# Performance work log

Hardware: AMD Instinct MI355X
Metric: run time of the kernel (lower is better)

## Reference

```python
import jax, jax.numpy as jnp
import numpy as np

D_MODEL = 4096
D_FIBER = 16
D_CONTROL = 64
EMA_MOMENTUM = 0.9


def setup_inputs() -> dict:
    key = jax.random.key(0)
    k_h, k_f, k_w1, k_w2 = jax.random.split(key, 4)
    B, S = 4, 2048
    hidden = jax.random.normal(k_h, (B, S, D_MODEL), dtype=jnp.float32)
    # torch nn.Linear stores weight as [out, in]; fiber_proj init: normal std=0.02
    W_fiber = jax.random.normal(k_f, (D_FIBER, D_MODEL), dtype=jnp.float32) * 0.02
    # predictor[0]: Linear(d_model+d_fiber, d_control) with default torch init (uniform)
    fan_in1 = D_MODEL + D_FIBER
    bound1 = 1.0 / np.sqrt(fan_in1)
    W1 = jax.random.uniform(k_w1, (D_CONTROL, fan_in1), dtype=jnp.float32, minval=-bound1, maxval=bound1)
    b1 = jnp.zeros((D_CONTROL,), dtype=jnp.float32)
    # predictor[-2]: Linear(d_control, 1), weight normal std=0.01, bias zero
    W2 = jax.random.normal(k_w2, (1, D_CONTROL), dtype=jnp.float32) * 0.01
    b2 = jnp.zeros((1,), dtype=jnp.float32)
    lam = jnp.asarray(1.0, dtype=jnp.float32)
    return {"hidden": hidden, "W_fiber": W_fiber, "W1": W1, "b1": b1, "W2": W2, "b2": b2, "lam": lam}


def _causal_ema(delta_h, alpha):
    # h_t = alpha*h_{t-1} + (1-alpha)*d_t, h_{-1} = 0. delta_h: [B,S]
    B = delta_h.shape[0]
    def step(h_prev, d_t):
        h_t = alpha * h_prev + (1.0 - alpha) * d_t
        return h_t, h_t
    _, hs = jax.lax.scan(step, jnp.zeros((B,), delta_h.dtype), jnp.swapaxes(delta_h, 0, 1))
    return jnp.swapaxes(hs, 0, 1)  # [B,S]


def reference(hidden, W_fiber, W1, b1, W2, b2, lam):
    h = hidden.astype(jnp.float32)                      # [B,S,D]
    fiber = jnp.einsum('bsd,fd->bsf', h, W_fiber)       # [B,S,16]
    combined = jnp.concatenate([h, fiber], axis=-1)     # [B,S,D+16]
    z = jax.nn.gelu(jnp.einsum('bsc,kc->bsk', combined, W1) + b1, approximate=False)
    delta_h = jax.nn.softplus(jnp.einsum('bsk,ok->bso', z, W2) + b2)[..., 0]  # [B,S]
    field = _causal_ema(delta_h, EMA_MOMENTUM)          # [B,S]
    gate = jax.nn.sigmoid(-lam * field)
    return gate.astype(hidden.dtype), field.astype(hidden.dtype), delta_h.mean()
```

## Files before the change

kernel.cpp:

```cpp
#include <hip/hip_runtime.h>
#include <hip/hip_bf16.h>

#define D_MODEL 4096
#define NTOK    8192
#define SEQ     2048

typedef short bf16x8 __attribute__((ext_vector_type(8)));
typedef float f32x4  __attribute__((ext_vector_type(4)));

__device__ __forceinline__ short f2bf(float x) {
  __hip_bfloat16 h = __float2bfloat16(x);
  return *reinterpret_cast<short*>(&h);
}
__device__ __forceinline__ float bfs2f(unsigned short u) {
  unsigned int x = ((unsigned int)u) << 16;
  float f;
  __builtin_memcpy(&f, &x, 4);
  return f;
}
__device__ __forceinline__ float bf2f(const void* p, size_t i) {
  return bfs2f(((const unsigned short*)p)[i]);
}

__device__ __forceinline__ void gload_lds16(const void* g, void* l) {
  __builtin_amdgcn_global_load_lds(
      (__attribute__((address_space(1))) void*)(g),
      (__attribute__((address_space(3))) void*)(l), 16, 0, 0);
}

__device__ __forceinline__ int sniff_wave(const unsigned short* p, int n) {
  int lane = threadIdx.x & 63;
  int S = n / 2 < 64 ? n / 2 : 64;
  bool act = lane < S;
  unsigned short ve = 0, vo = 0;
  if (act) { ve = p[2 * lane]; vo = p[2 * lane + 1]; }
  int ee = (ve >> 7) & 0xFF, eo = (vo >> 7) & 0xFF;
  bool ve_band   = (ve == 0) || (ve == 0x8000) || (ee >= 96 && ee <= 141);
  bool vo_bandnz = (vo != 0) && (vo != 0x8000) && (eo >= 96 && eo <= 141);
  int zp = __popcll(__ballot(act && ve == 0 && vo == 0));
  int ob = __popcll(__ballot(act && ve == 0 && vo_bandnz));
  int eb = __popcll(__ballot(act && ve_band));
  if (zp == S) return 1;
  if (4 * ob >= 3 * S) return 0;
  if (4 * eb >= 3 * S) return 1;
  return 0;
}

__device__ __forceinline__ float decode_lam(const void* lamp) {
  unsigned short l0 = *(const unsigned short*)lamp;
  int le = (l0 >> 7) & 0xFF;
  if (l0 != 0 && l0 != 0x8000 && le >= 96 && le <= 141)
    return bfs2f(l0);
  return *(const float*)lamp;
}
__device__ __forceinline__ float decode_b2(const void* p) {
  unsigned short c0 = *(const unsigned short*)p;
  int ce = (c0 >> 7) & 0xFF;
  if (c0 == 0) return 0.0f;
  if (c0 != 0x8000 && ce >= 96 && ce <= 141)
    return bfs2f(c0);
  return *(const float*)p;
}

__global__ __launch_bounds__(256) void fold_w1(const void* __restrict__ W1v,
                                               const void* __restrict__ Wfv,
                                               short* __restrict__ W1eff) {
  int n = blockIdx.x;
  int fw1 = sniff_wave((const unsigned short*)W1v, 64 * 4112);
  int fwf = sniff_wave((const unsigned short*)Wfv, 16 * D_MODEL);
  __shared__ float w1b[16];
  if (threadIdx.x < 16) {
    size_t idx = (size_t)n * 4112 + 4096 + threadIdx.x;
    w1b[threadIdx.x] = fw1 ? bf2f(W1v, idx) : ((const float*)W1v)[idx];
  }
  __syncthreads();
  for (int it = 0; it < 4; ++it) {
    int k0 = it * 1024 + threadIdx.x * 4;
    size_t idx = (size_t)n * 4112 + k0;
    float v0, v1, v2, v3;
    if (fw1) {
      ushort4 u = *(const ushort4*)((const unsigned short*)W1v + idx);
      v0 = bfs2f(u.x); v1 = bfs2f(u.y); v2 = bfs2f(u.z); v3 = bfs2f(u.w);
    } else {
      float4 f = *(const float4*)((const float*)W1v + idx);
      v0 = f.x; v1 = f.y; v2 = f.z; v3 = f.w;
    }
#pragma unroll
    for (int f = 0; f < 16; ++f) {
      size_t wi = (size_t)f * D_MODEL + k0;
      float w0, w1_, w2_, w3_;
      if (fwf) {
        ushort4 u = *(const ushort4*)((const unsigned short*)Wfv + wi);
        w0 = bfs2f(u.x); w1_ = bfs2f(u.y); w2_ = bfs2f(u.z); w3_ = bfs2f(u.w);
      } else {
        float4 fv = *(const float4*)((const float*)Wfv + wi);
        w0 = fv.x; w1_ = fv.y; w2_ = fv.z; w3_ = fv.w;
      }
      float s = w1b[f];
      v0 += s * w0; v1 += s * w1_; v2 += s * w2_; v3 += s * w3_;
    }
    ushort4 o;
    o.x = (unsigned short)f2bf(v0); o.y = (unsigned short)f2bf(v1);
    o.z = (unsigned short)f2bf(v2); o.w = (unsigned short)f2bf(v3);
    *(ushort4*)(W1eff + (size_t)n * D_MODEL + k0) = o;
  }
}

__global__ __launch_bounds__(256, 2) void gemm_part(const void* __restrict__ hid,
                                                    const short* __restrict__ B_,
                                                    float* __restrict__ part) {
  int t = blockIdx.x >> 3;
  int c = blockIdx.x & 7;
  int w    = threadIdx.x >> 6;
  int lane = threadIdx.x & 63;
  int m = lane & 15, kg = lane >> 4;

  __shared__ short As[64 * 512];

  int fhid = sniff_wave((const unsigned short*)hid, NTOK * D_MODEL);

  f32x4 acc0 = {0.f, 0.f, 0.f, 0.f};
  f32x4 acc1 = acc0, acc2 = acc0, acc3 = acc0;

  const short* Bp = B_ + (size_t)m * D_MODEL + c * 512 + kg * 8;

  if (fhid) {
#pragma unroll
    for (int i = 0; i < 16; ++i) {
      int n = w * 16 + i;
      const char* src = (const char*)hid +
          ((size_t)(t * 64 + n) * D_MODEL + c * 512) * 2 +
          ((lane ^ (n & 7)) * 16);
      gload_lds16(src, (char*)As + n * 1024);
    }
    asm volatile("s_waitcnt vmcnt(0)" ::: "memory");
#pragma unroll
    for (int s = 0; s < 16; ++s) {
      int u  = s * 4 + kg;
      int row = w * 16 + m;
      bf16x8 a = *(const bf16x8*)((const char*)As + row * 1024 +
                                  ((u ^ (m & 7)) * 16));
      bf16x8 b0 = *(const bf16x8*)(Bp + (size_t)0 * 16 * D_MODEL + s * 32);
      bf16x8 b1 = *(const bf16x8*)(Bp + (size_t)1 * 16 * D_MODEL + s * 32);
      bf16x8 b2 = *(const bf16x8*)(Bp + (size_t)2 * 16 * D_MODEL + s * 32);
      bf16x8 b3 = *(const bf16x8*)(Bp + (size_t)3 * 16 * D_MODEL + s * 32);
      acc0 = __builtin_amdgcn_mfma_f32_16x16x32_bf16(a, b0, acc0, 0, 0, 0);
      acc1 = __builtin_amdgcn_mfma_f32_16x16x32_bf16(a, b1, acc1, 0, 0, 0);
      acc2 = __builtin_amdgcn_mfma_f32_16x16x32_bf16(a, b2, acc2, 0, 0, 0);
      acc3 = __builtin_amdgcn_mfma_f32_16x16x32_bf16(a, b3, acc3, 0, 0, 0);
    }
  } else {
    const float* Ap = (const float*)hid +
        (size_t)(t * 64 + w * 16 + m) * D_MODEL + c * 512 + kg * 8;
    for (int s = 0; s < 16; ++s) {
      float4 lo = *(const float4*)(Ap + s * 32);
      float4 hi = *(const float4*)(Ap + s * 32 + 4);
      bf16x8 a;
      a[0] = f2bf(lo.x); a[1] = f2bf(lo.y); a[2] = f2bf(lo.z); a[3] = f2bf(lo.w);
      a[4] = f2bf(hi.x); a[5] = f2bf(hi.y); a[6] = f2bf(hi.z); a[7] = f2bf(hi.w);
      bf16x8 b0 = *(const bf16x8*)(Bp + (size_t)0 * 16 * D_MODEL + s * 32);
      bf16x8 b1 = *(const bf16x8*)(Bp + (size_t)1 * 16 * D_MODEL + s * 32);
      bf16x8 b2 = *(const bf16x8*)(Bp + (size_t)2 * 16 * D_MODEL + s * 32);
      bf16x8 b3 = *(const bf16x8*)(Bp + (size_t)3 * 16 * D_MODEL + s * 32);
      acc0 = __builtin_amdgcn_mfma_f32_16x16x32_bf16(a, b0, acc0, 0, 0, 0);
      acc1 = __builtin_amdgcn_mfma_f32_16x16x32_bf16(a, b1, acc1, 0, 0, 0);
      acc2 = __builtin_amdgcn_mfma_f32_16x16x32_bf16(a, b2, acc2, 0, 0, 0);
      acc3 = __builtin_amdgcn_mfma_f32_16x16x32_bf16(a, b3, acc3, 0, 0, 0);
    }
  }

  float* po = part + ((size_t)c * NTOK + (size_t)t * 64 + w * 16) * 64;
#pragma unroll
  for (int r = 0; r < 4; ++r) {
    int row = kg * 4 + r;
    po[row * 64 + (m +  0)] = acc0[r];
    po[row * 64 + (m + 16)] = acc1[r];
    po[row * 64 + (m + 32)] = acc2[r];
    po[row * 64 + (m + 48)] = acc3[r];
  }
}

__global__ __launch_bounds__(256) void delta_ep(const float* __restrict__ part,
                                                const void* __restrict__ b1,
                                                const void* __restrict__ w2,
                                                const void* __restrict__ b2p,
                                                float* __restrict__ delta) {
  int tok = blockIdx.x * 16 + (threadIdx.x >> 4);
  int cid = threadIdx.x & 15;
  int fb1 = sniff_wave((const unsigned short*)b1, 64);
  int fw2 = sniff_wave((const unsigned short*)w2, 64);
  float y = 0.f;
#pragma unroll
  for (int j = 0; j < 4; ++j) {
    int col = cid + 16 * j;
    float s = 0.f;
#pragma unroll
    for (int c = 0; c < 8; ++c)
      s += part[((size_t)c * NTOK + tok) * 64 + col];
    s += fb1 ? bf2f(b1, col) : ((const float*)b1)[col];
    float g = 0.5f * s * (1.0f + erff(s * 0.70710678118654752f));
    y += g * (fw2 ? bf2f(w2, col) : ((const float*)w2)[col]);
  }
#pragma unroll
  for (int off = 1; off <= 8; off <<= 1) y += __shfl_xor(y, off, 64);
  if (cid == 0) {
    float x = y + decode_b2(b2p);
    float d = (x > 20.0f) ? x : log1pf(expf(x));
    delta[tok] = d;
  }
}

__global__ __launch_bounds__(256) void ema_out(const float* __restrict__ delta,
                                               const void* __restrict__ lamp,
                                               float* __restrict__ out) {
  int b    = threadIdx.x >> 6;
  int lane = threadIdx.x & 63;
  const float alpha = 0.9f;
  float d[32];
  const float* dp = delta + b * SEQ + lane * 32;
  float beta = 0.f, lsum = 0.f;
#pragma unroll
  for (int i = 0; i < 32; ++i) {
    d[i] = dp[i];
    lsum += d[i];
    beta = alpha * beta + 0.1f * d[i];
  }
  float accA = 0.03433683820292512f;
  float accB = beta;
  for (int off = 1; off < 64; off <<= 1) {
    float uA = __shfl_up(accA, off, 64);
    float uB = __shfl_up(accB, off, 64);
    if (lane >= off) {
      accB = accB + accA * uB;
      accA = accA * uA;
    }
  }
  float prev = __shfl_up(accB, 1, 64);
  float h = (lane == 0) ? 0.f : prev;
  float lam = decode_lam(lamp);
#pragma unroll
  for (int i = 0; i < 32; ++i) {
    h = alpha * h + 0.1f * d[i];
    float gate = 1.0f / (1.0f + expf(lam * h));
    out[b * SEQ + lane * 32 + i]        = gate;
    out[NTOK + b * SEQ + lane * 32 + i] = h;
  }
#pragma unroll
  for (int off = 32; off >= 1; off >>= 1) lsum += __shfl_xor(lsum, off, 64);
  __shared__ float bs[4];
  if (lane == 0) bs[b] = lsum;
  __syncthreads();
  if (threadIdx.x == 0)
    out[2 * NTOK] = (bs[0] + bs[1] + bs[2] + bs[3]) * (1.0f / 8192.0f);
}

extern "C" void kernel_launch(void* const* d_in, const int* in_sizes, int n_in,
                              void* d_out, int out_size, void* d_ws, size_t ws_size,
                              hipStream_t stream) {
  const void* hidden = d_in[0];
  const void* Wf     = d_in[1];
  const void* W1     = d_in[2];
  const void* b1     = d_in[3];
  const void* W2     = d_in[4];
  const void* b2     = d_in[5];
  const void* lam    = d_in[6];
  float* out = (float*)d_out;

  char* ws = (char*)d_ws;
  short* W1eff = (short*)ws;
  float* delta = (float*)(ws + (size_t)64 * D_MODEL * 2);
  float* part  = (float*)(ws + (size_t)64 * D_MODEL * 2 + NTOK * 4);

  fold_w1<<<64, 256, 0, stream>>>(W1, Wf, W1eff);
  gemm_part<<<1024, 256, 0, stream>>>(hidden, W1eff, part);
  delta_ep<<<512, 256, 0, stream>>>(part, b1, W2, b2, delta);
  ema_out<<<1, 256, 0, stream>>>(delta, lam, out);
}
```

Before: 227.2 us.

## Split K into sixteen chunks and stage folded weights in LDS

The GEMM's K dimension is now split into 16 chunks of 256 instead of 8 chunks of 512, doubling the grid to 2048 blocks for more parallelism. Each block also stages its 64x256 slice of the folded W1 into a swizzled LDS buffer, so all four waves share one copy instead of each re-reading it from global memory. The cost is twice the partial-sum traffic to and from the workspace, a 64KB LDS footprint per block, and a workspace requirement that may outgrow the allocated buffer.

```diff
diff --git a/kernel.cpp b/kernel.cpp
--- a/kernel.cpp
+++ b/kernel.cpp
@@ -4,6 +4,8 @@
 #define D_MODEL 4096
 #define NTOK    8192
 #define SEQ     2048
+#define NCHUNK  16
+#define KC      256
 
 typedef short bf16x8 __attribute__((ext_vector_type(8)));
 typedef float f32x4  __attribute__((ext_vector_type(4)));
@@ -109,41 +111,52 @@
 __global__ __launch_bounds__(256, 2) void gemm_part(const void* __restrict__ hid,
                                                     const short* __restrict__ B_,
                                                     float* __restrict__ part) {
-  int t = blockIdx.x >> 3;
-  int c = blockIdx.x & 7;
+  int t = blockIdx.x >> 4;
+  int c = blockIdx.x & 15;
   int w    = threadIdx.x >> 6;
   int lane = threadIdx.x & 63;
   int m = lane & 15, kg = lane >> 4;
 
-  __shared__ short As[64 * 512];
+  __shared__ char smem[65536];
+  char* As  = smem;
+  char* Bsm = smem + 32768;
 
   int fhid = sniff_wave((const unsigned short*)hid, NTOK * D_MODEL);
+
+#pragma unroll
+  for (int j = 0; j < 8; ++j) {
+    int row = w * 16 + 2 * j + (lane >> 5);
+    const char* src = (const char*)B_ + (size_t)row * (D_MODEL * 2) + c * 512 +
+                      (((lane & 31) ^ (row & 7)) * 16);
+    gload_lds16(src, Bsm + w * 8192 + j * 1024);
+  }
+
+  if (fhid) {
+#pragma unroll
+    for (int i = 0; i < 8; ++i) {
+      int row = w * 16 + 2 * i + (lane >> 5);
+      const char* src = (const char*)hid +
+          ((size_t)(t * 64 + row) * D_MODEL + c * KC) * 2 +
+          (((lane & 31) ^ (row & 7)) * 16);
+      gload_lds16(src, As + w * 8192 + i * 1024);
+    }
+  }
+  asm volatile("s_waitcnt vmcnt(0)" ::: "memory");
+  __syncthreads();
 
   f32x4 acc0 = {0.f, 0.f, 0.f, 0.f};
   f32x4 acc1 = acc0, acc2 = acc0, acc3 = acc0;
 
-  const short* Bp = B_ + (size_t)m * D_MODEL + c * 512 + kg * 8;
-
   if (fhid) {
 #pragma unroll
-    for (int i = 0; i < 16; ++i) {
-      int n = w * 16 + i;
-      const char* src = (const char*)hid +
-          ((size_t)(t * 64 + n) * D_MODEL + c * 512) * 2 +
-          ((lane ^ (n & 7)) * 16);
-      gload_lds16(src, (char*)As + n * 1024);
-    }
-    asm volatile("s_waitcnt vmcnt(0)" ::: "memory");
-#pragma unroll
-    for (int s = 0; s < 16; ++s) {
+    for (int s = 0; s < 8; ++s) {
       int u  = s * 4 + kg;
-      int row = w * 16 + m;
-      bf16x8 a = *(const bf16x8*)((const char*)As + row * 1024 +
-                                  ((u ^ (m & 7)) * 16));
-      bf16x8 b0 = *(const bf16x8*)(Bp + (size_t)0 * 16 * D_MODEL + s * 32);
-      bf16x8 b1 = *(const bf16x8*)(Bp + (size_t)1 * 16 * D_MODEL + s * 32);
-      bf16x8 b2 = *(const bf16x8*)(Bp + (size_t)2 * 16 * D_MODEL + s * 32);
-      bf16x8 b3 = *(const bf16x8*)(Bp + (size_t)3 * 16 * D_MODEL + s * 32);
+      int sw = ((u ^ (m & 7)) * 16);
+      bf16x8 a  = *(const bf16x8*)(As  + w * 8192 + m * 512 + sw);
+      bf16x8 b0 = *(const bf16x8*)(Bsm + 0 * 8192 + m * 512 + sw);
+      bf16x8 b1 = *(const bf16x8*)(Bsm + 1 * 8192 + m * 512 + sw);
+      bf16x8 b2 = *(const bf16x8*)(Bsm + 2 * 8192 + m * 512 + sw);
+      bf16x8 b3 = *(const bf16x8*)(Bsm + 3 * 8192 + m * 512 + sw);
       acc0 = __builtin_amdgcn_mfma_f32_16x16x32_bf16(a, b0, acc0, 0, 0, 0);
       acc1 = __builtin_amdgcn_mfma_f32_16x16x32_bf16(a, b1, acc1, 0, 0, 0);
       acc2 = __builtin_amdgcn_mfma_f32_16x16x32_bf16(a, b2, acc2, 0, 0, 0);
@@ -151,17 +164,19 @@
     }
   } else {
     const float* Ap = (const float*)hid +
-        (size_t)(t * 64 + w * 16 + m) * D_MODEL + c * 512 + kg * 8;
-    for (int s = 0; s < 16; ++s) {
+        (size_t)(t * 64 + w * 16 + m) * D_MODEL + c * KC + kg * 8;
+    for (int s = 0; s < 8; ++s) {
       float4 lo = *(const float4*)(Ap + s * 32);
       float4 hi = *(const float4*)(Ap + s * 32 + 4);
       bf16x8 a;
       a[0] = f2bf(lo.x); a[1] = f2bf(lo.y); a[2] = f2bf(lo.z); a[3] = f2bf(lo.w);
       a[4] = f2bf(hi.x); a[5] = f2bf(hi.y); a[6] = f2bf(hi.z); a[7] = f2bf(hi.w);
-      bf16x8 b0 = *(const bf16x8*)(Bp + (size_t)0 * 16 * D_MODEL + s * 32);
-      bf16x8 b1 = *(const bf16x8*)(Bp + (size_t)1 * 16 * D_MODEL + s * 32);
-      bf16x8 b2 = *(const bf16x8*)(Bp + (size_t)2 * 16 * D_MODEL + s * 32);
-      bf16x8 b3 = *(const bf16x8*)(Bp + (size_t)3 * 16 * D_MODEL + s * 32);
+      int u  = s * 4 + kg;
+      int sw = ((u ^ (m & 7)) * 16);
+      bf16x8 b0 = *(const bf16x8*)(Bsm + 0 * 8192 + m * 512 + sw);
+      bf16x8 b1 = *(const bf16x8*)(Bsm + 1 * 8192 + m * 512 + sw);
+      bf16x8 b2 = *(const bf16x8*)(Bsm + 2 * 8192 + m * 512 + sw);
+      bf16x8 b3 = *(const bf16x8*)(Bsm + 3 * 8192 + m * 512 + sw);
       acc0 = __builtin_amdgcn_mfma_f32_16x16x32_bf16(a, b0, acc0, 0, 0, 0);
       acc1 = __builtin_amdgcn_mfma_f32_16x16x32_bf16(a, b1, acc1, 0, 0, 0);
       acc2 = __builtin_amdgcn_mfma_f32_16x16x32_bf16(a, b2, acc2, 0, 0, 0);
@@ -195,7 +210,7 @@
     int col = cid + 16 * j;
     float s = 0.f;
 #pragma unroll
-    for (int c = 0; c < 8; ++c)
+    for (int c = 0; c < NCHUNK; ++c)
       s += part[((size_t)c * NTOK + tok) * 64 + col];
     s += fb1 ? bf2f(b1, col) : ((const float*)b1)[col];
     float g = 0.5f * s * (1.0f + erff(s * 0.70710678118654752f));
@@ -272,7 +287,7 @@
   float* part  = (float*)(ws + (size_t)64 * D_MODEL * 2 + NTOK * 4);
 
   fold_w1<<<64, 256, 0, stream>>>(W1, Wf, W1eff);
-  gemm_part<<<1024, 256, 0, stream>>>(hidden, W1eff, part);
+  gemm_part<<<2048, 256, 0, stream>>>(hidden, W1eff, part);
   delta_ep<<<512, 256, 0, stream>>>(part, b1, W2, b2, delta);
   ema_out<<<1, 256, 0, stream>>>(delta, lam, out);
 }
```

After: 228.1 us. Within noise of the previous version (+0.4%).
